# Optimization experiments

Measured on AMD Instinct MI355X. Metric: run time of the kernel, lower is better.

Reference implementation:

```python
import jax, jax.numpy as jnp
import numpy as np

NUM_HEADS = 16
HEAD_DIM = 64  # d_out // num_heads


def setup_inputs() -> dict:
    key = jax.random.key(0)
    ks = jax.random.split(key, 6)
    d_in, d_out, b, t = 1024, 1024, 2, 2048
    s = 0.02
    return {
        "x": jax.random.normal(ks[0], (b, t, d_in), jnp.float32),
        "Wq": jax.random.normal(ks[1], (d_in, d_out), jnp.float32) * s,
        "Wk": jax.random.normal(ks[2], (d_in, d_out), jnp.float32) * s,
        "Wv": jax.random.normal(ks[3], (d_in, d_out), jnp.float32) * s,
        "Wo": jax.random.normal(ks[4], (d_out, d_out), jnp.float32) * s,
        "bo": jnp.zeros((d_out,), jnp.float32),
    }


def reference(x, Wq, Wk, Wv, Wo, bo):
    b, t, _ = x.shape
    H, hd = NUM_HEADS, HEAD_DIM
    # qkv projections (no bias), split into heads: [b, H, t, hd]
    q = (x @ Wq).reshape(b, t, H, hd).transpose(0, 2, 1, 3)
    k = (x @ Wk).reshape(b, t, H, hd).transpose(0, 2, 1, 3)
    v = (x @ Wv).reshape(b, t, H, hd).transpose(0, 2, 1, 3)
    # raw scores, causal mask (masked_fill with -1e9 BEFORE the 1/sqrt(hd) scale,
    # matching the source exactly), then scaled softmax
    scores = jnp.einsum("bhqd,bhkd->bhqk", q, k)
    causal = jnp.triu(jnp.ones((t, t), dtype=bool), k=1)
    scores = jnp.where(causal[None, None], jnp.float32(-1e9), scores)
    attn = jax.nn.softmax(scores / jnp.sqrt(jnp.float32(hd)), axis=-1)
    # dropout is identity in eval mode
    ctx = jnp.einsum("bhqk,bhkd->bhqd", attn, v)  # [b, H, t, hd]
    ctx = ctx.transpose(0, 2, 1, 3).reshape(b, t, H * hd)
    return ctx @ Wo + bo
```

## Files before the change

### kernel.cpp

```cpp
#include <hip/hip_runtime.h>


#define SEQ   2048
#define DMODEL 1024
#define NH    16
#define HD    64
#define MROWS 4096

typedef __attribute__((ext_vector_type(4))) float f32x4;
typedef __attribute__((ext_vector_type(16))) float f32x16;
typedef __attribute__((ext_vector_type(8))) short short8;
typedef __attribute__((ext_vector_type(4))) unsigned int u32x4;

#define MFMA16(a, b, c) __builtin_amdgcn_mfma_f32_16x16x32_bf16((a), (b), (c), 0, 0, 0)
#define MFMA32(a, b, c) __builtin_amdgcn_mfma_f32_32x32x16_bf16((a), (b), (c), 0, 0, 0)

__device__ __forceinline__ unsigned short f2bf(float f) {
  union { float f; unsigned u; } v; v.f = f;
  return (unsigned short)((v.u + 0x7fffu + ((v.u >> 16) & 1u)) >> 16);
}

__device__ __forceinline__ float exp2x(float x) {
#if __has_builtin(__builtin_amdgcn_exp2f)
  return __builtin_amdgcn_exp2f(x);
#else
  float r; asm("v_exp_f32 %0, %1" : "=v"(r) : "v"(x)); return r;
#endif
}

__device__ __forceinline__ unsigned cvt_pk(float lo, float hi) {
  unsigned r;
  asm volatile("v_cvt_pk_bf16_f32 %0, %1, %2" : "=v"(r) : "v"(lo), "v"(hi));
  return r;
}

__device__ __forceinline__ void pls(unsigned& a, unsigned& b) {
  asm("v_permlane32_swap_b32 %0, %1" : "+v"(a), "+v"(b));
}

__device__ __forceinline__ short8 as_short8(u32x4 v) {
  union { u32x4 u; short8 s; } x; x.u = v; return x.s;
}

__device__ __forceinline__ f32x4 zero4() {
  f32x4 z; z[0] = 0.f; z[1] = 0.f; z[2] = 0.f; z[3] = 0.f; return z;
}

__device__ __forceinline__ void async16(const void* g, void* l) {
  __builtin_amdgcn_global_load_lds(
      (const __attribute__((address_space(1))) unsigned int*)g,
      (__attribute__((address_space(3))) unsigned int*)l, 16, 0, 0);
}

__global__ __launch_bounds__(256) void prep(
    const float* __restrict__ x, const float* __restrict__ Wq,
    const float* __restrict__ Wk, const float* __restrict__ Wv,
    const float* __restrict__ Wo, unsigned short* __restrict__ xb,
    unsigned short* __restrict__ Wt, unsigned short* __restrict__ WoT) {
  __shared__ unsigned short tile[64][65];
  const int bx = blockIdx.x;
  if (bx < 2048) {
    int i = bx * 256 + threadIdx.x;
    const float4* p = (const float4*)x;
    float4 a = p[2 * i];
    float4 b = p[2 * i + 1];
    short8 o;
    o[0] = (short)f2bf(a.x); o[1] = (short)f2bf(a.y);
    o[2] = (short)f2bf(a.z); o[3] = (short)f2bf(a.w);
    o[4] = (short)f2bf(b.x); o[5] = (short)f2bf(b.y);
    o[6] = (short)f2bf(b.z); o[7] = (short)f2bf(b.w);
    *(short8*)&xb[(size_t)i * 8] = o;
    return;
  }
  const int id2 = bx - 2048;
  const int m = id2 >> 8;
  const float* W = (m == 0) ? Wq : (m == 1) ? Wk : (m == 2) ? Wv : Wo;
  unsigned short* D = (m == 3) ? WoT : Wt + (size_t)m * 1024 * 1024;
  const int tid = id2 & 255;
  const int kb = (tid >> 4) * 64, nb = (tid & 15) * 64;
  const int t = threadIdx.x;
  const int tx = t & 63, ty = t >> 6;
#pragma unroll
  for (int rr = 0; rr < 16; rr++) {
    int r = ty * 16 + rr;
    tile[r][tx] = f2bf(W[(size_t)(kb + r) * 1024 + nb + tx]);
  }
  __syncthreads();
#pragma unroll
  for (int rr = 0; rr < 16; rr++) {
    int r = ty * 16 + rr;
    D[(size_t)(nb + r) * 1024 + kb + tx] = tile[tx][r];
  }
}

template <int MODE, int WMF>
__global__ __launch_bounds__(256) void gemm_bt(
    const unsigned short* __restrict__ A, const unsigned short* __restrict__ Bt,
    unsigned short* __restrict__ Qo, unsigned short* __restrict__ Ko,
    unsigned short* __restrict__ Vo, float* __restrict__ out,
    const float* __restrict__ bo) {
  constexpr int K = 1024;
  constexpr int BM = WMF * 32;
  constexpr int NW = K / 64;
  constexpr int ASZ = BM * 32;
  constexpr int BSZ = 128 * 32;
  __shared__ __align__(16) unsigned short smem[4 * ASZ + 4 * BSZ];
  unsigned short* Asb = smem;
  unsigned short* Bsb = smem + 4 * ASZ;
  const int t = threadIdx.x;
  const int lane = t & 63;
  const int w = t >> 6;
  const int lr = lane & 15, kf = lane >> 4;
  const int wr = w >> 1, wc = w & 1;

  const int nwg = gridDim.x * gridDim.y;
  const int id = blockIdx.y * gridDim.x + blockIdx.x;
  const int swz = (id & 7) * (nwg >> 3) + (id >> 3);
  const int bx = swz % gridDim.x, by = swz / gridDim.x;

  const int rowbase = bx * BM;
  const int colbase = by * 128;

  const unsigned short* Ab = A + (size_t)rowbase * K;
  const unsigned short* Bb = Bt + (size_t)colbase * K;

  f32x4 acc[WMF][4];
#pragma unroll
  for (int m = 0; m < WMF; m++)
#pragma unroll
    for (int n = 0; n < 4; n++) acc[m][n] = zero4();

  auto stage = [&](int buf, int wi) {
#pragma unroll
    for (int sub = 0; sub < 2; sub++) {
      int k0 = (2 * wi + sub) * 32;
      unsigned short* Ad = Asb + ((size_t)buf * 2 + sub) * ASZ;
      unsigned short* Bd = Bsb + ((size_t)buf * 2 + sub) * BSZ;
#pragma unroll
      for (int i = 0; i < BM / 64; i++) {
        int f = i * 256 + t;
        int c = f ^ ((f >> 3) & 3);
        int row = c >> 2;
        int col = (c & 3) << 3;
        async16(Ab + (size_t)row * K + k0 + col, (char*)Ad + (size_t)f * 16);
      }
#pragma unroll
      for (int i = 0; i < 2; i++) {
        int f = i * 256 + t;
        int c = f ^ ((f >> 3) & 3);
        int row = c >> 2;
        int col = (c & 3) << 3;
        async16(Bb + (size_t)row * K + k0 + col, (char*)Bd + (size_t)f * 16);
      }
    }
  };

  auto compute = [&](int buf, int sub) {
    const unsigned short* As = Asb + ((size_t)buf * 2 + sub) * ASZ;
    const unsigned short* Bs = Bsb + ((size_t)buf * 2 + sub) * BSZ;
    short8 av[WMF], bv[4];
#pragma unroll
    for (int m = 0; m < WMF; m++) {
      int row = wr * (WMF * 16) + m * 16 + lr;
      int idx = (row * 32 + kf * 8) ^ (((row >> 1) & 3) << 3);
      av[m] = *(const short8*)&As[idx];
    }
#pragma unroll
    for (int n = 0; n < 4; n++) {
      int row = wc * 64 + n * 16 + lr;
      int idx = (row * 32 + kf * 8) ^ (((row >> 1) & 3) << 3);
      bv[n] = *(const short8*)&Bs[idx];
    }
    __builtin_amdgcn_s_setprio(1);
#pragma unroll
    for (int m = 0; m < WMF; m++)
#pragma unroll
      for (int n = 0; n < 4; n++) acc[m][n] = MFMA16(av[m], bv[n], acc[m][n]);
    __builtin_amdgcn_s_setprio(0);
  };

  stage(0, 0);
  int cur = 0;

  for (int wi = 0; wi < NW; wi++) {
    if (wi + 1 < NW) {
      stage(cur ^ 1, wi + 1);
      if constexpr (MODE == 0) asm volatile("s_waitcnt vmcnt(8)" ::: "memory");
      else                     asm volatile("s_waitcnt vmcnt(6)" ::: "memory");
    } else {
      asm volatile("s_waitcnt vmcnt(0)" ::: "memory");
    }
    __builtin_amdgcn_s_barrier();

    compute(cur, 0);
    compute(cur, 1);

    __builtin_amdgcn_s_barrier();
    cur ^= 1;
  }

  if constexpr (MODE == 0) {
    if (colbase < 2048) {
      const int selq = colbase >> 10;
      unsigned short* dst = selq ? Ko : Qo;
      const float sc = selq ? 1.0f : 0.18033688011112042f;
#pragma unroll
      for (int n = 0; n < 4; n++) {
        int c = colbase + wc * 64 + n * 16 + lr;
        int hh = (c >> 6) & 15;
        int dd = c & 63;
#pragma unroll
        for (int m = 0; m < WMF; m++) {
          int r0 = rowbase + wr * (WMF * 16) + m * 16 + kf * 4;
#pragma unroll
          for (int i = 0; i < 4; i++) {
            int r = r0 + i;
            int bi = r >> 11;
            int tq = r & 2047;
            dst[((size_t)(bi * NH + hh) * SEQ + tq) * HD + dd] = f2bf(acc[m][n][i] * sc);
          }
        }
      }
    } else {
      unsigned short* tr = smem;
#pragma unroll
      for (int n = 0; n < 4; n++) {
        int ccol = wc * 64 + n * 16 + lr;
#pragma unroll
        for (int m = 0; m < WMF; m++) {
#pragma unroll
          for (int i = 0; i < 4; i++) {
            int rrow = wr * (WMF * 16) + m * 16 + kf * 4 + i;
            tr[ccol * 136 + rrow] = f2bf(acc[m][n][i]);
          }
        }
      }
      __syncthreads();
      const int bi2 = rowbase >> 11;
      const int tq0 = rowbase & 2047;
#pragma unroll
      for (int k2 = 0; k2 < 8; k2++) {
        int u = k2 * 256 + t;
        int cc = u >> 4, seg = u & 15;
        int c = colbase + cc;
        int hh = (c >> 6) & 15, dd = c & 63;
        short8 v8 = *(const short8*)&tr[cc * 136 + seg * 8];
        *(short8*)&Vo[((size_t)(bi2 * NH + hh) * HD + dd) * SEQ + tq0 + seg * 8] = v8;
      }
    }
  } else {
#pragma unroll
    for (int n = 0; n < 4; n++) {
      int c = colbase + wc * 64 + n * 16 + lr;
      float bias = bo[c];
#pragma unroll
      for (int m = 0; m < WMF; m++) {
        int r0 = rowbase + wr * (WMF * 16) + m * 16 + kf * 4;
#pragma unroll
        for (int i = 0; i < 4; i++) {
          out[(size_t)(r0 + i) * 1024 + c] = acc[m][n][i] + bias;
        }
      }
    }
  }
}

__global__ __launch_bounds__(256) void attn_fwd(
    const unsigned short* __restrict__ Q, const unsigned short* __restrict__ K,
    const unsigned short* __restrict__ Vt, unsigned short* __restrict__ ctx) {
  const int bh = blockIdx.x;
  const int y = blockIdx.y;
  const int qt = (y < 8) ? (15 - y) : (y - 8);
  const int bi = bh >> 4, hh = bh & 15;
  const int t = threadIdx.x, lane = t & 63, w = t >> 6;
  const int qc = lane & 31, hi = lane >> 5;

  __shared__ __align__(16) unsigned short Ks[2][2][64 * 64];
  __shared__ __align__(16) unsigned short Vs[2][2][64 * 64];

  const unsigned short* Qb = Q + (size_t)bh * SEQ * HD;
  const unsigned short* Kb = K + (size_t)bh * SEQ * HD;
  const unsigned short* Vb = Vt + (size_t)bh * HD * SEQ;

  const int qrow = qt * 128 + w * 32;
  short8 qv[4];
#pragma unroll
  for (int c = 0; c < 4; c++)
    qv[c] = *(const short8*)&Qb[(size_t)(qrow + qc) * HD + c * 16 + hi * 8];

  f32x16 o0, o1;
#pragma unroll
  for (int i = 0; i < 16; i++) { o0[i] = 0.f; o1[i] = 0.f; }
  float l_acc = 0.f;

  const int ktmax = 2 * qt + (w >> 1);
  const int NP = qt + 1;

  auto stage = [&](int buf, int p) {
#pragma unroll
    for (int sub = 0; sub < 2; sub++) {
      int kt = 2 * p + sub;
#pragma unroll
      for (int i2 = 0; i2 < 2; i2++) {
        int f = i2 * 256 + t;
        int c = f ^ ((f >> 3) & 7);
        async16(Kb + (size_t)kt * 64 * HD + (size_t)c * 8,
                (char*)&Ks[buf][sub][0] + (size_t)f * 16);
        int d = c >> 3, ko = (c & 7) << 3;
        async16(Vb + (size_t)d * SEQ + (size_t)kt * 64 + ko,
                (char*)&Vs[buf][sub][0] + (size_t)f * 16);
      }
    }
  };

  auto qk = [&](const unsigned short* Kt, f32x16& s0, f32x16& s1) {
#pragma unroll
    for (int i = 0; i < 16; i++) { s0[i] = 0.f; s1[i] = 0.f; }
    __builtin_amdgcn_s_setprio(1);
#pragma unroll
    for (int c = 0; c < 4; c++) {
      int i0 = (qc * 64 + c * 16 + hi * 8) ^ ((qc & 7) << 3);
      s0 = MFMA32(*(const short8*)&Kt[i0], qv[c], s0);
      int r1 = 32 + qc;
      int i1 = (r1 * 64 + c * 16 + hi * 8) ^ ((r1 & 7) << 3);
      s1 = MFMA32(*(const short8*)&Kt[i1], qv[c], s1);
    }
    __builtin_amdgcn_s_setprio(0);
  };

  auto maskit = [&](f32x16& s0, f32x16& s1, int kt) {
    const int qg = qrow + qc;
#pragma unroll
    for (int reg = 0; reg < 16; reg++) {
      int rloc = (reg & 3) + 8 * (reg >> 2) + 4 * hi;
      int kg = kt * 64 + rloc;
      if (kg > qg) s0[reg] = -1e30f;
      if (kg + 32 > qg) s1[reg] = -1e30f;
    }
  };

  auto smpack = [&](const f32x16& s0, const f32x16& s1, unsigned* w0, unsigned* w1) {
    float psA = 0.f, psB = 0.f;
#pragma unroll
    for (int j = 0; j < 8; j++) {
      float a0 = exp2x(s0[2 * j]), b0 = exp2x(s0[2 * j + 1]);
      float a1 = exp2x(s1[2 * j]), b1 = exp2x(s1[2 * j + 1]);
      psA += a0 + b0;
      psB += a1 + b1;
      w0[j] = cvt_pk(a0, b0);
      w1[j] = cvt_pk(a1, b1);
    }
    l_acc += psA + psB;
  };

  auto pv = [&](const unsigned short* Vtile, unsigned* w0, unsigned* w1) {
    __builtin_amdgcn_s_setprio(1);
#pragma unroll
    for (int h2 = 0; h2 < 2; h2++) {
      unsigned* pw = h2 ? w1 : w0;
#pragma unroll
      for (int cc = 0; cc < 2; cc++) {
        unsigned a0 = pw[cc * 4 + 0], b0 = pw[cc * 4 + 2];
        unsigned a1 = pw[cc * 4 + 1], b1 = pw[cc * 4 + 3];
        pls(a0, b0);
        pls(a1, b1);
        u32x4 pf; pf[0] = a0; pf[1] = a1; pf[2] = b0; pf[3] = b1;
        short8 pfrag = as_short8(pf);
        int c2 = h2 * 2 + cc;
        int ia = (qc * 64 + c2 * 16 + hi * 8) ^ ((qc & 7) << 3);
        o0 = MFMA32(*(const short8*)&Vtile[ia], pfrag, o0);
        int rb = 32 + qc;
        int ib = (rb * 64 + c2 * 16 + hi * 8) ^ ((rb & 7) << 3);
        o1 = MFMA32(*(const short8*)&Vtile[ib], pfrag, o1);
      }
    }
    __builtin_amdgcn_s_setprio(0);
  };

  stage(0, 0);
  int cur = 0;

  for (int p = 0; p < NP; p++) {
    if (p + 1 < NP) {
      stage(cur ^ 1, p + 1);
      asm volatile("s_waitcnt vmcnt(8)" ::: "memory");
    } else {
      asm volatile("s_waitcnt vmcnt(0)" ::: "memory");
    }
    __builtin_amdgcn_s_barrier();

    const bool v0 = (2 * p <= ktmax);
    const bool v1 = (2 * p + 1 <= ktmax);
    f32x16 sA0, sA1, sB0, sB1;
    if (v0) qk(&Ks[cur][0][0], sA0, sA1);
    if (v1) qk(&Ks[cur][1][0], sB0, sB1);
    if (v0 && 2 * p == ktmax)     maskit(sA0, sA1, 2 * p);
    if (v1 && 2 * p + 1 == ktmax) maskit(sB0, sB1, 2 * p + 1);
    unsigned w0A[8], w1A[8], w0B[8], w1B[8];
    if (v0) smpack(sA0, sA1, w0A, w1A);
    if (v1) smpack(sB0, sB1, w0B, w1B);
    if (v0) pv(&Vs[cur][0][0], w0A, w1A);
    if (v1) pv(&Vs[cur][1][0], w0B, w1B);

    __builtin_amdgcn_s_barrier();
    cur ^= 1;
  }

  float l = l_acc + __shfl_xor(l_acc, 32);
  float inv = 1.0f / l;
  const size_t rowoff = ((size_t)bi * SEQ + qrow + qc) * DMODEL + hh * HD;
#pragma unroll
  for (int g = 0; g < 4; g++) {
    unsigned pa = cvt_pk(o0[4 * g] * inv, o0[4 * g + 1] * inv);
    unsigned pb = cvt_pk(o0[4 * g + 2] * inv, o0[4 * g + 3] * inv);
    uint2 vv; vv.x = pa; vv.y = pb;
    *(uint2*)&ctx[rowoff + 8 * g + 4 * hi] = vv;
    unsigned pc = cvt_pk(o1[4 * g] * inv, o1[4 * g + 1] * inv);
    unsigned pd = cvt_pk(o1[4 * g + 2] * inv, o1[4 * g + 3] * inv);
    uint2 ww; ww.x = pc; ww.y = pd;
    *(uint2*)&ctx[rowoff + 32 + 8 * g + 4 * hi] = ww;
  }
}

extern "C" void kernel_launch(void* const* d_in, const int* in_sizes, int n_in,
                              void* d_out, int out_size, void* d_ws, size_t ws_size,
                              hipStream_t stream) {
  const float* x  = (const float*)d_in[0];
  const float* Wq = (const float*)d_in[1];
  const float* Wk = (const float*)d_in[2];
  const float* Wv = (const float*)d_in[3];
  const float* Wo = (const float*)d_in[4];
  const float* bo = (const float*)d_in[5];
  float* out = (float*)d_out;

  unsigned short* xb   = (unsigned short*)d_ws;
  unsigned short* Wt   = xb + (size_t)MROWS * DMODEL;
  unsigned short* WoT  = Wt + (size_t)3 * 1024 * 1024;
  unsigned short* Qb   = WoT + (size_t)1024 * 1024;
  unsigned short* Kb   = Qb + (size_t)MROWS * DMODEL;
  unsigned short* Vb   = Kb + (size_t)MROWS * DMODEL;
  unsigned short* ctxb = Vb + (size_t)MROWS * DMODEL;

  prep<<<3072, 256, 0, stream>>>(x, Wq, Wk, Wv, Wo, xb, Wt, WoT);

  gemm_bt<0, 4><<<dim3(32, 24), 256, 0, stream>>>(xb, Wt, Qb, Kb, Vb, nullptr, nullptr);
  attn_fwd<<<dim3(32, 16), 256, 0, stream>>>(Qb, Kb, Vb, ctxb);
  gemm_bt<1, 2><<<dim3(64, 8), 256, 0, stream>>>(ctxb, WoT, nullptr, nullptr, nullptr, out, bo);
}
```

Measured before the change: 103.6 us.

## Balance causal attention by pairing complementary query tiles in one 512-thread block

Each block now handles two query tiles, qa=15-y and qb=y, using two 256-thread groups. Every group processes exactly 9 key-pair steps: group 0 does the first 8 pairs of tile A, and group 1 does all of tile B and then the rest of tile A. The two partial results for tile A are merged through shared memory before writing. This removes the load imbalance of the causal triangle across blocks and halves the grid. The cost is double the shared memory per block, more registers for two accumulator sets, and an extra reduction step at the end.

```diff
diff --git a/kernel.cpp b/kernel.cpp
--- a/kernel.cpp
+++ b/kernel.cpp
@@ -265,36 +265,49 @@
   }
 }
 
-__global__ __launch_bounds__(256) void attn_fwd(
+__global__ __launch_bounds__(512) void attn_fwd(
     const unsigned short* __restrict__ Q, const unsigned short* __restrict__ K,
     const unsigned short* __restrict__ Vt, unsigned short* __restrict__ ctx) {
   const int bh = blockIdx.x;
   const int y = blockIdx.y;
-  const int qt = (y < 8) ? (15 - y) : (y - 8);
+  const int qa = 15 - y, qb = y;
   const int bi = bh >> 4, hh = bh & 15;
   const int t = threadIdx.x, lane = t & 63, w = t >> 6;
+  const int g = w >> 2, wl = w & 3, tg = t & 255;
   const int qc = lane & 31, hi = lane >> 5;
 
-  __shared__ __align__(16) unsigned short Ks[2][2][64 * 64];
-  __shared__ __align__(16) unsigned short Vs[2][2][64 * 64];
+  __shared__ __align__(16) unsigned short Ks[2][2][2][4096];
+  __shared__ __align__(16) unsigned short Vs[2][2][2][4096];
 
   const unsigned short* Qb = Q + (size_t)bh * SEQ * HD;
   const unsigned short* Kb = K + (size_t)bh * SEQ * HD;
   const unsigned short* Vb = Vt + (size_t)bh * HD * SEQ;
 
-  const int qrow = qt * 128 + w * 32;
-  short8 qv[4];
+  const int qrowA = qa * 128 + wl * 32;
+  const int qrowB = qb * 128 + wl * 32;
+  const int ktmaxA = 2 * qa + (wl >> 1);
+  const int ktmaxB = 2 * qb + (wl >> 1);
+
+  short8 qvA[4], qvB[4];
 #pragma unroll
   for (int c = 0; c < 4; c++)
-    qv[c] = *(const short8*)&Qb[(size_t)(qrow + qc) * HD + c * 16 + hi * 8];
-
-  f32x16 o0, o1;
-#pragma unroll
-  for (int i = 0; i < 16; i++) { o0[i] = 0.f; o1[i] = 0.f; }
-  float l_acc = 0.f;
-
-  const int ktmax = 2 * qt + (w >> 1);
-  const int NP = qt + 1;
+    qvA[c] = *(const short8*)&Qb[(size_t)(qrowA + qc) * HD + c * 16 + hi * 8];
+  if (g == 1) {
+#pragma unroll
+    for (int c = 0; c < 4; c++)
+      qvB[c] = *(const short8*)&Qb[(size_t)(qrowB + qc) * HD + c * 16 + hi * 8];
+  }
+
+  f32x16 oA0, oA1, oB0, oB1;
+#pragma unroll
+  for (int i = 0; i < 16; i++) { oA0[i] = 0.f; oA1[i] = 0.f; oB0[i] = 0.f; oB1[i] = 0.f; }
+  float lA = 0.f, lB = 0.f;
+
+  auto pairAt = [&](int i, bool& useB, int& p) -> bool {
+    if (g == 0) { useB = false; p = i; return i < 8; }
+    if (i <= qb) { useB = true; p = i; return true; }
+    useB = false; p = 8 + (i - qb - 1); return true;
+  };
 
   auto stage = [&](int buf, int p) {
 #pragma unroll
@@ -302,18 +315,18 @@
       int kt = 2 * p + sub;
 #pragma unroll
       for (int i2 = 0; i2 < 2; i2++) {
-        int f = i2 * 256 + t;
+        int f = i2 * 256 + tg;
         int c = f ^ ((f >> 3) & 7);
         async16(Kb + (size_t)kt * 64 * HD + (size_t)c * 8,
-                (char*)&Ks[buf][sub][0] + (size_t)f * 16);
+                (char*)&Ks[g][buf][sub][0] + (size_t)f * 16);
         int d = c >> 3, ko = (c & 7) << 3;
         async16(Vb + (size_t)d * SEQ + (size_t)kt * 64 + ko,
-                (char*)&Vs[buf][sub][0] + (size_t)f * 16);
-      }
-    }
-  };
-
-  auto qk = [&](const unsigned short* Kt, f32x16& s0, f32x16& s1) {
+                (char*)&Vs[g][buf][sub][0] + (size_t)f * 16);
+      }
+    }
+  };
+
+  auto qk = [&](const unsigned short* Kt, const short8* qv, f32x16& s0, f32x16& s1) {
 #pragma unroll
     for (int i = 0; i < 16; i++) { s0[i] = 0.f; s1[i] = 0.f; }
     __builtin_amdgcn_s_setprio(1);
@@ -328,7 +341,7 @@
     __builtin_amdgcn_s_setprio(0);
   };
 
-  auto maskit = [&](f32x16& s0, f32x16& s1, int kt) {
+  auto maskit = [&](f32x16& s0, f32x16& s1, int kt, int qrow) {
     const int qg = qrow + qc;
 #pragma unroll
     for (int reg = 0; reg < 16; reg++) {
@@ -339,7 +352,8 @@
     }
   };
 
-  auto smpack = [&](const f32x16& s0, const f32x16& s1, unsigned* w0, unsigned* w1) {
+  auto smpack = [&](const f32x16& s0, const f32x16& s1, unsigned* w0, unsigned* w1,
+                    float& lacc) {
     float psA = 0.f, psB = 0.f;
 #pragma unroll
     for (int j = 0; j < 8; j++) {
@@ -350,10 +364,11 @@
       w0[j] = cvt_pk(a0, b0);
       w1[j] = cvt_pk(a1, b1);
     }
-    l_acc += psA + psB;
-  };
-
-  auto pv = [&](const unsigned short* Vtile, unsigned* w0, unsigned* w1) {
+    lacc += psA + psB;
+  };
+
+  auto pv = [&](const unsigned short* Vtile, unsigned* w0, unsigned* w1,
+                f32x16& o0, f32x16& o1) {
     __builtin_amdgcn_s_setprio(1);
 #pragma unroll
     for (int h2 = 0; h2 < 2; h2++) {
@@ -377,48 +392,108 @@
     __builtin_amdgcn_s_setprio(0);
   };
 
-  stage(0, 0);
+  auto do_pair = [&](int cur, int p, const short8* qv, int ktmax, int qrow,
+                     f32x16& o0, f32x16& o1, float& lacc) {
+    const bool v0 = (2 * p <= ktmax);
+    const bool v1 = (2 * p + 1 <= ktmax);
+    f32x16 sA0, sA1, sB0, sB1;
+    if (v0) qk(&Ks[g][cur][0][0], qv, sA0, sA1);
+    if (v1) qk(&Ks[g][cur][1][0], qv, sB0, sB1);
+    if (v0 && 2 * p == ktmax)     maskit(sA0, sA1, 2 * p, qrow);
+    if (v1 && 2 * p + 1 == ktmax) maskit(sB0, sB1, 2 * p + 1, qrow);
+    unsigned w0A[8], w1A[8], w0B[8], w1B[8];
+    if (v0) smpack(sA0, sA1, w0A, w1A, lacc);
+    if (v1) smpack(sB0, sB1, w0B, w1B, lacc);
+    if (v0) pv(&Vs[g][cur][0][0], w0A, w1A, o0, o1);
+    if (v1) pv(&Vs[g][cur][1][0], w0B, w1B, o0, o1);
+  };
+
+  {
+    bool ub; int p0;
+    if (pairAt(0, ub, p0)) stage(0, p0);
+  }
   int cur = 0;
 
-  for (int p = 0; p < NP; p++) {
-    if (p + 1 < NP) {
-      stage(cur ^ 1, p + 1);
+  for (int i = 0; i < 9; i++) {
+    bool ubn; int pn;
+    const bool hasn = (i + 1 < 9) && pairAt(i + 1, ubn, pn);
+    if (hasn) {
+      stage(cur ^ 1, pn);
       asm volatile("s_waitcnt vmcnt(8)" ::: "memory");
     } else {
       asm volatile("s_waitcnt vmcnt(0)" ::: "memory");
     }
     __builtin_amdgcn_s_barrier();
 
-    const bool v0 = (2 * p <= ktmax);
-    const bool v1 = (2 * p + 1 <= ktmax);
-    f32x16 sA0, sA1, sB0, sB1;
-    if (v0) qk(&Ks[cur][0][0], sA0, sA1);
-    if (v1) qk(&Ks[cur][1][0], sB0, sB1);
-    if (v0 && 2 * p == ktmax)     maskit(sA0, sA1, 2 * p);
-    if (v1 && 2 * p + 1 == ktmax) maskit(sB0, sB1, 2 * p + 1);
-    unsigned w0A[8], w1A[8], w0B[8], w1B[8];
-    if (v0) smpack(sA0, sA1, w0A, w1A);
-    if (v1) smpack(sB0, sB1, w0B, w1B);
-    if (v0) pv(&Vs[cur][0][0], w0A, w1A);
-    if (v1) pv(&Vs[cur][1][0], w0B, w1B);
+    bool ub; int p;
+    if (pairAt(i, ub, p)) {
+      if (ub) do_pair(cur, p, qvB, ktmaxB, qrowB, oB0, oB1, lB);
+      else    do_pair(cur, p, qvA, ktmaxA, qrowA, oA0, oA1, lA);
+    }
 
     __builtin_amdgcn_s_barrier();
     cur ^= 1;
   }
 
-  float l = l_acc + __shfl_xor(l_acc, 32);
-  float inv = 1.0f / l;
-  const size_t rowoff = ((size_t)bi * SEQ + qrow + qc) * DMODEL + hh * HD;
-#pragma unroll
-  for (int g = 0; g < 4; g++) {
-    unsigned pa = cvt_pk(o0[4 * g] * inv, o0[4 * g + 1] * inv);
-    unsigned pb = cvt_pk(o0[4 * g + 2] * inv, o0[4 * g + 3] * inv);
-    uint2 vv; vv.x = pa; vv.y = pb;
-    *(uint2*)&ctx[rowoff + 8 * g + 4 * hi] = vv;
-    unsigned pc = cvt_pk(o1[4 * g] * inv, o1[4 * g + 1] * inv);
-    unsigned pd = cvt_pk(o1[4 * g + 2] * inv, o1[4 * g + 3] * inv);
-    uint2 ww; ww.x = pc; ww.y = pd;
-    *(uint2*)&ctx[rowoff + 32 + 8 * g + 4 * hi] = ww;
+  float* ex = (float*)&Ks[0][0][0][0];
+  float* lex = ex + 128 * 65;
+
+  float lApart = lA + __shfl_xor(lA, 32);
+
+  __builtin_amdgcn_s_barrier();
+  if (g == 1) {
+    const int row = wl * 32 + qc;
+#pragma unroll
+    for (int gi = 0; gi < 4; gi++) {
+#pragma unroll
+      for (int jj = 0; jj < 4; jj++) {
+        ex[row * 65 + 8 * gi + 4 * hi + jj] = oA0[4 * gi + jj];
+        ex[row * 65 + 32 + 8 * gi + 4 * hi + jj] = oA1[4 * gi + jj];
+      }
+    }
+    if (hi == 0) lex[row] = lApart;
+  }
+  __builtin_amdgcn_s_barrier();
+
+  if (g == 0) {
+    const int row = wl * 32 + qc;
+#pragma unroll
+    for (int gi = 0; gi < 4; gi++) {
+#pragma unroll
+      for (int jj = 0; jj < 4; jj++) {
+        oA0[4 * gi + jj] += ex[row * 65 + 8 * gi + 4 * hi + jj];
+        oA1[4 * gi + jj] += ex[row * 65 + 32 + 8 * gi + 4 * hi + jj];
+      }
+    }
+    float l = lApart + lex[row];
+    float inv = 1.0f / l;
+    const size_t rowoff = ((size_t)bi * SEQ + qrowA + qc) * DMODEL + hh * HD;
+#pragma unroll
+    for (int gi = 0; gi < 4; gi++) {
+      unsigned pa = cvt_pk(oA0[4 * gi] * inv, oA0[4 * gi + 1] * inv);
+      unsigned pb = cvt_pk(oA0[4 * gi + 2] * inv, oA0[4 * gi + 3] * inv);
+      uint2 vv; vv.x = pa; vv.y = pb;
+      *(uint2*)&ctx[rowoff + 8 * gi + 4 * hi] = vv;
+      unsigned pc = cvt_pk(oA1[4 * gi] * inv, oA1[4 * gi + 1] * inv);
+      unsigned pd = cvt_pk(oA1[4 * gi + 2] * inv, oA1[4 * gi + 3] * inv);
+      uint2 ww; ww.x = pc; ww.y = pd;
+      *(uint2*)&ctx[rowoff + 32 + 8 * gi + 4 * hi] = ww;
+    }
+  } else {
+    float l = lB + __shfl_xor(lB, 32);
+    float inv = 1.0f / l;
+    const size_t rowoff = ((size_t)bi * SEQ + qrowB + qc) * DMODEL + hh * HD;
+#pragma unroll
+    for (int gi = 0; gi < 4; gi++) {
+      unsigned pa = cvt_pk(oB0[4 * gi] * inv, oB0[4 * gi + 1] * inv);
+      unsigned pb = cvt_pk(oB0[4 * gi + 2] * inv, oB0[4 * gi + 3] * inv);
+      uint2 vv; vv.x = pa; vv.y = pb;
+      *(uint2*)&ctx[rowoff + 8 * gi + 4 * hi] = vv;
+      unsigned pc = cvt_pk(oB1[4 * gi] * inv, oB1[4 * gi + 1] * inv);
+      unsigned pd = cvt_pk(oB1[4 * gi + 2] * inv, oB1[4 * gi + 3] * inv);
+      uint2 ww; ww.x = pc; ww.y = pd;
+      *(uint2*)&ctx[rowoff + 32 + 8 * gi + 4 * hi] = ww;
+    }
   }
 }
 
@@ -444,6 +519,6 @@
   prep<<<3072, 256, 0, stream>>>(x, Wq, Wk, Wv, Wo, xb, Wt, WoT);
 
   gemm_bt<0, 4><<<dim3(32, 24), 256, 0, stream>>>(xb, Wt, Qb, Kb, Vb, nullptr, nullptr);
-  attn_fwd<<<dim3(32, 16), 256, 0, stream>>>(Qb, Kb, Vb, ctxb);
+  attn_fwd<<<dim3(32, 8), 512, 0, stream>>>(Qb, Kb, Vb, ctxb);
   gemm_bt<1, 2><<<dim3(64, 8), 256, 0, stream>>>(ctxb, WoT, nullptr, nullptr, nullptr, out, bo);
 }
```

After: 98.29 us, median of 2. 5.1% less time.
